# Optimization experiments

Measured on AMD Instinct MI355X. Metric: run time of the kernel, lower is better.

Reference implementation:

```python
import jax, jax.numpy as jnp
import numpy as np

DIM_BODY = 10
DIM_OBJECT = 15
NB_OBJECTS = 3
FIRST_INDS = np.array([0,1,2,3,4,5,6,7,8,9,10,11,12,13,15,16,17,20,21,25])
SECOND_INDS = np.array([0,1,2,3,4,5,6,7,8,9,14,18,19,22,23,24,26,27,28,29])
LOG_SIG_MIN, LOG_SIG_MAX = -20.0, 2.0


def setup_inputs() -> dict:
    key = jax.random.key(0)
    ks = jax.random.split(key, 16)
    B = 65536
    s = 0.05  # weight scale, keeps activations sane
    return {
        "obs": jax.random.normal(ks[0], (B, DIM_BODY + NB_OBJECTS * DIM_OBJECT), jnp.float32),
        "ag": jax.random.normal(ks[1], (B, 30), jnp.float32),
        "g": jax.random.normal(ks[2], (B, 30), jnp.float32),
        "phi_w1": jax.random.normal(ks[3], (80, 256), jnp.float32) * s,
        "phi_b1": jnp.zeros((256,), jnp.float32),
        "phi_w2": jax.random.normal(ks[4], (256, 256), jnp.float32) * s,
        "phi_b2": jnp.zeros((256,), jnp.float32),
        "rho_w1": jax.random.normal(ks[5], (256, 256), jnp.float32) * s,
        "rho_b1": jnp.zeros((256,), jnp.float32),
        "mean_w": jax.random.normal(ks[6], (256, 4), jnp.float32) * s,
        "mean_b": jnp.zeros((4,), jnp.float32),
        "logstd_w": jax.random.normal(ks[7], (256, 4), jnp.float32) * s,
        "logstd_b": jnp.zeros((4,), jnp.float32),
    }


def reference(obs, ag, g, phi_w1, phi_b1, phi_w2, phi_b2, rho_w1, rho_b1,
              mean_w, mean_b, logstd_w, logstd_b):
    body = obs[:, :DIM_BODY]  # [B,10]
    objs = [obs[:, DIM_BODY + DIM_OBJECT * i: DIM_BODY + DIM_OBJECT * (i + 1)]
            for i in range(NB_OBJECTS)]
    ag_f, g_f = ag[:, FIRST_INDS], g[:, FIRST_INDS]
    ag_s, g_s = ag[:, SECOND_INDS], g[:, SECOND_INDS]
    pair_inputs = []
    for i in range(NB_OBJECTS):
        for j in range(NB_OBJECTS):
            if i < j:
                pair_inputs.append(jnp.concatenate([ag_f, body, g_f, objs[i], objs[j]], axis=1))
            elif j < i:
                pair_inputs.append(jnp.concatenate([ag_s, body, g_s, objs[i], objs[j]], axis=1))
    inp = jnp.stack(pair_inputs)  # [6, B, 80]
    # shared phi MLP (2 layers, ReLU on both)
    h = jax.nn.relu(jnp.einsum('pbi,ih->pbh', inp, phi_w1) + phi_b1)
    phi = jax.nn.relu(jnp.einsum('pbh,ho->pbo', h, phi_w2) + phi_b2)
    agg = phi.sum(axis=0)  # [B, 256] sum over pairs
    # rho head
    hr = jax.nn.relu(agg @ rho_w1 + rho_b1)
    mean = hr @ mean_w + mean_b
    logstd = jnp.clip(hr @ logstd_w + logstd_b, LOG_SIG_MIN, LOG_SIG_MAX)
    return mean, logstd
```

## Files before the change

kernel.cpp:

```cpp
#include <hip/hip_runtime.h>
#include <hip/hip_bf16.h>


#define B_TOTAL 65536
#define TROWS   64
#define RSTR    136

typedef __attribute__((ext_vector_type(8))) short s8v;
typedef __attribute__((ext_vector_type(4))) float f4v;

__constant__ int c_PI[6] = {0,0,1,1,2,2};
__constant__ int c_PJ[6] = {1,2,0,2,0,1};
__constant__ int c_PF[6] = {0,0,1,0,1,1};
__constant__ int c_INV[2][30] = {
  {0,1,2,3,4,5,6,7,8,9,10,11,12,13,-1,14,15,16,-1,-1,17,18,-1,-1,-1,19,-1,-1,-1,-1},
  {0,1,2,3,4,5,6,7,8,9,-1,-1,-1,-1,10,-1,-1,-1,11,12,-1,-1,13,14,15,-1,16,17,18,19}};

static __device__ __forceinline__ short bf16s(float v) {
  __hip_bfloat16 h = __float2bfloat16(v);
  union { __hip_bfloat16 h; short s; } u; u.h = h; return u.s;
}

__global__ __launch_bounds__(256)
void prep_weights(const float* __restrict__ phi_w1,
                  const float* __restrict__ phi_b1,
                  const float* __restrict__ phi_w2,
                  const float* __restrict__ rho_w1,
                  const float* __restrict__ mean_w,
                  const float* __restrict__ logstd_w,
                  __hip_bfloat16* __restrict__ W1P,
                  __hip_bfloat16* __restrict__ W2f,
                  __hip_bfloat16* __restrict__ W3f,
                  __hip_bfloat16* __restrict__ W4f) {
  const int wid  = (blockIdx.x * blockDim.x + threadIdx.x) >> 6;
  const int lane = threadIdx.x & 63;
  const int l15  = lane & 15;
  const int kq   = (lane >> 4) * 8;
  if (wid >= 648) return;
  union { short s[8]; s8v v; } o;
  __hip_bfloat16* dst;
  if (wid < 384) {
    const int p = wid >> 6, rem = wid & 63;
    const int nb = rem >> 2, ks = rem & 3;
    const int n = nb * 16 + l15;
    const int f = c_PF[p], oi = c_PI[p], oj = c_PJ[p];
#pragma unroll
    for (int j = 0; j < 8; ++j) {
      int k = ks * 32 + kq + j;
      float v = 0.0f;
      if (k < 30)       { int t = c_INV[f][k];      if (t >= 0) v = phi_w1[t * 256 + n]; }
      else if (k < 60)  { int t = c_INV[f][k - 30]; if (t >= 0) v = phi_w1[(30 + t) * 256 + n]; }
      else if (k < 70)  { v = phi_w1[(20 + k - 60) * 256 + n]; }
      else if (k < 115) { int q = (k - 70) / 15, t = (k - 70) - q * 15;
                          int c = (q == oi) ? 50 + t : (q == oj) ? 65 + t : -1;
                          if (c >= 0) v = phi_w1[c * 256 + n]; }
      else if (k == 115) v = phi_b1[n];
      o.s[j] = bf16s(v);
    }
    dst = W1P + wid * 512 + lane * 8;
  } else if (wid < 512) {
    const int r = wid - 384;
    const int nb = r >> 3, ks = r & 7;
    const int n = nb * 16 + l15;
#pragma unroll
    for (int j = 0; j < 8; ++j)
      o.s[j] = bf16s(phi_w2[(ks * 32 + kq + j) * 256 + n]);
    dst = W2f + r * 512 + lane * 8;
  } else if (wid < 640) {
    const int r = wid - 512;
    const int nb = r >> 3, ks = r & 7;
    const int n = nb * 16 + l15;
#pragma unroll
    for (int j = 0; j < 8; ++j)
      o.s[j] = bf16s(rho_w1[(ks * 32 + kq + j) * 256 + n]);
    dst = W3f + r * 512 + lane * 8;
  } else {
    const int ks = wid - 640;
    const int n = l15;
#pragma unroll
    for (int j = 0; j < 8; ++j) {
      int k = ks * 32 + kq + j;
      float v = (n < 4) ? mean_w[k * 4 + n]
              : (n < 8) ? logstd_w[k * 4 + (n - 4)] : 0.0f;
      o.s[j] = bf16s(v);
    }
    dst = W4f + ks * 512 + lane * 8;
  }
  *reinterpret_cast<s8v*>(dst) = o.v;
}

static __device__ __forceinline__ unsigned pk2(float a, float b) {
  __hip_bfloat162 h = __float22bfloat162_rn(float2{a, b});
  union { __hip_bfloat162 h2; unsigned u; } cv; cv.h2 = h;
  return cv.u;
}

__global__ __launch_bounds__(512, 2)
void actor_main(const float* __restrict__ obs, const float* __restrict__ ag,
                const float* __restrict__ g,
                const __hip_bfloat16* __restrict__ W1P,
                const __hip_bfloat16* __restrict__ W2f,
                const __hip_bfloat16* __restrict__ W3f,
                const __hip_bfloat16* __restrict__ W4f,
                const float* __restrict__ b2, const float* __restrict__ b3,
                const float* __restrict__ meanb,
                const float* __restrict__ logstdb,
                float* __restrict__ out) {
  __shared__ __align__(16) __hip_bfloat16 rawS[TROWS * RSTR];
  __shared__ __align__(16) __hip_bfloat16 HsBuf[2][4 * 8 * 512];

  const int tid  = threadIdx.x;
  const int lane = tid & 63;
  const int w    = tid >> 6;
  const int l15  = lane & 15;
  const int quad = lane >> 4;
  const int r0   = blockIdx.x * TROWS;

  float4 b2v[2];
#pragma unroll
  for (int i = 0; i < 2; ++i)
    b2v[i] = *(const float4*)&b2[w * 32 + i * 16 + quad * 4];

  s8v w2f[8][2];
#pragma unroll
  for (int i = 0; i < 2; ++i)
#pragma unroll
    for (int ks = 0; ks < 8; ++ks)
      w2f[ks][i] = *(const s8v*)&W2f[(((w * 2 + i) * 8 + ks) * 512) + lane * 8];

  {
    const int row = tid >> 3;
    const int c0  = (tid & 7) * 16;
    const float* agr = ag  + (size_t)(r0 + row) * 30;
    const float* gr  = g   + (size_t)(r0 + row) * 30;
    const float* obr = obs + (size_t)(r0 + row) * 55;
    union { short s[16]; s8v v[2]; } o;
#pragma unroll
    for (int cc = 0; cc < 16; ++cc) {
      int c = c0 + cc;
      float v;
      if      (c < 30)  v = agr[c];
      else if (c < 60)  v = gr[c - 30];
      else if (c < 115) v = obr[c - 60];
      else if (c == 115) v = 1.0f;
      else              v = 0.0f;
      o.s[cc] = bf16s(v);
    }
    *reinterpret_cast<s8v*>(&rawS[row * RSTR + c0])     = o.v[0];
    *reinterpret_cast<s8v*>(&rawS[row * RSTR + c0 + 8]) = o.v[1];
  }

  s8v w1c[4][2], w1n[4][2];
#pragma unroll
  for (int i = 0; i < 2; ++i)
#pragma unroll
    for (int ks = 0; ks < 4; ++ks)
      w1c[ks][i] = *(const s8v*)&W1P[(((w * 2 + i) * 4 + ks) * 512) + lane * 8];

  f4v agg[2][4];
#pragma unroll
  for (int i = 0; i < 2; ++i)
#pragma unroll
    for (int rt = 0; rt < 4; ++rt) agg[i][rt] = f4v{0.f, 0.f, 0.f, 0.f};

  const int ebase = l15 * 8 + (quad >> 1) * 128 + (quad & 1) * 4;

  __syncthreads();

#pragma unroll 1
  for (int p = 0; p < 6; ++p) {
    __hip_bfloat16* buf = &HsBuf[p & 1][0];

    if (p < 5) {
      const __hip_bfloat16* nb = W1P + (p + 1) * 32768;
#pragma unroll
      for (int i = 0; i < 2; ++i)
#pragma unroll
        for (int ks = 0; ks < 4; ++ks)
          w1n[ks][i] = *(const s8v*)&nb[(((w * 2 + i) * 4 + ks) * 512) + lane * 8];
    }

    f4v h[2][4];
#pragma unroll
    for (int i = 0; i < 2; ++i)
#pragma unroll
      for (int rt = 0; rt < 4; ++rt) h[i][rt] = f4v{0.f, 0.f, 0.f, 0.f};
#pragma unroll
    for (int ks = 0; ks < 4; ++ks) {
      s8v bx[4];
#pragma unroll
      for (int rt = 0; rt < 4; ++rt)
        bx[rt] = *(const s8v*)&rawS[(rt * 16 + l15) * RSTR + ks * 32 + quad * 8];
#pragma unroll
      for (int i = 0; i < 2; ++i)
#pragma unroll
        for (int rt = 0; rt < 4; ++rt)
          h[i][rt] = __builtin_amdgcn_mfma_f32_16x16x32_bf16(w1c[ks][i], bx[rt], h[i][rt], 0, 0, 0);
    }
#pragma unroll
    for (int i = 0; i < 2; ++i)
#pragma unroll
      for (int rt = 0; rt < 4; ++rt) {
        float v0 = fmaxf(h[i][rt][0], 0.f);
        float v1 = fmaxf(h[i][rt][1], 0.f);
        float v2 = fmaxf(h[i][rt][2], 0.f);
        float v3 = fmaxf(h[i][rt][3], 0.f);
        uint2 U; U.x = pk2(v0, v1); U.y = pk2(v2, v3);
        *reinterpret_cast<uint2*>(&buf[(rt * 8 + w) * 512 + i * 256 + ebase]) = U;
      }
    __syncthreads();

    f4v a2[2][4];
#pragma unroll
    for (int i = 0; i < 2; ++i)
#pragma unroll
      for (int rt = 0; rt < 4; ++rt) a2[i][rt] = f4v{0.f, 0.f, 0.f, 0.f};
#pragma unroll
    for (int ks = 0; ks < 8; ++ks) {
      s8v hf[4];
#pragma unroll
      for (int rt = 0; rt < 4; ++rt)
        hf[rt] = *(const s8v*)&buf[(rt * 8 + ks) * 512 + lane * 8];
#pragma unroll
      for (int i = 0; i < 2; ++i)
#pragma unroll
        for (int rt = 0; rt < 4; ++rt)
          a2[i][rt] = __builtin_amdgcn_mfma_f32_16x16x32_bf16(w2f[ks][i], hf[rt], a2[i][rt], 0, 0, 0);
    }
#pragma unroll
    for (int i = 0; i < 2; ++i)
#pragma unroll
      for (int rt = 0; rt < 4; ++rt) {
        agg[i][rt][0] += fmaxf(a2[i][rt][0] + b2v[i].x, 0.f);
        agg[i][rt][1] += fmaxf(a2[i][rt][1] + b2v[i].y, 0.f);
        agg[i][rt][2] += fmaxf(a2[i][rt][2] + b2v[i].z, 0.f);
        agg[i][rt][3] += fmaxf(a2[i][rt][3] + b2v[i].w, 0.f);
      }

    if (p < 5) {
#pragma unroll
      for (int i = 0; i < 2; ++i)
#pragma unroll
        for (int ks = 0; ks < 4; ++ks)
          w1c[ks][i] = w1n[ks][i];
    }
  }

  s8v w3f[8][2];
#pragma unroll
  for (int i = 0; i < 2; ++i)
#pragma unroll
    for (int ks = 0; ks < 8; ++ks)
      w3f[ks][i] = *(const s8v*)&W3f[(((w * 2 + i) * 8 + ks) * 512) + lane * 8];
  float4 b3v[2];
#pragma unroll
  for (int i = 0; i < 2; ++i)
    b3v[i] = *(const float4*)&b3[w * 32 + i * 16 + quad * 4];

  {
    __hip_bfloat16* bufA = &HsBuf[0][0];
#pragma unroll
    for (int i = 0; i < 2; ++i)
#pragma unroll
      for (int rt = 0; rt < 4; ++rt) {
        uint2 U; U.x = pk2(agg[i][rt][0], agg[i][rt][1]);
        U.y = pk2(agg[i][rt][2], agg[i][rt][3]);
        *reinterpret_cast<uint2*>(&bufA[(rt * 8 + w) * 512 + i * 256 + ebase]) = U;
      }
  }
  __syncthreads();

  f4v a3[2][4];
#pragma unroll
  for (int i = 0; i < 2; ++i)
#pragma unroll
    for (int rt = 0; rt < 4; ++rt) a3[i][rt] = f4v{0.f, 0.f, 0.f, 0.f};
  {
    const __hip_bfloat16* bufA = &HsBuf[0][0];
#pragma unroll
    for (int ks = 0; ks < 8; ++ks) {
      s8v hf[4];
#pragma unroll
      for (int rt = 0; rt < 4; ++rt)
        hf[rt] = *(const s8v*)&bufA[(rt * 8 + ks) * 512 + lane * 8];
#pragma unroll
      for (int i = 0; i < 2; ++i)
#pragma unroll
        for (int rt = 0; rt < 4; ++rt)
          a3[i][rt] = __builtin_amdgcn_mfma_f32_16x16x32_bf16(w3f[ks][i], hf[rt], a3[i][rt], 0, 0, 0);
    }
  }
  {
    __hip_bfloat16* bufB = &HsBuf[1][0];
#pragma unroll
    for (int i = 0; i < 2; ++i)
#pragma unroll
      for (int rt = 0; rt < 4; ++rt) {
        float v0 = fmaxf(a3[i][rt][0] + b3v[i].x, 0.f);
        float v1 = fmaxf(a3[i][rt][1] + b3v[i].y, 0.f);
        float v2 = fmaxf(a3[i][rt][2] + b3v[i].z, 0.f);
        float v3 = fmaxf(a3[i][rt][3] + b3v[i].w, 0.f);
        uint2 U; U.x = pk2(v0, v1); U.y = pk2(v2, v3);
        *reinterpret_cast<uint2*>(&bufB[(rt * 8 + w) * 512 + i * 256 + ebase]) = U;
      }
  }
  __syncthreads();

  if (w < 4) {
    const __hip_bfloat16* bufB = &HsBuf[1][0];
    f4v a4 = f4v{0.f, 0.f, 0.f, 0.f};
#pragma unroll
    for (int ks = 0; ks < 8; ++ks) {
      s8v w4 = *(const s8v*)&W4f[ks * 512 + lane * 8];
      s8v hf = *(const s8v*)&bufB[(w * 8 + ks) * 512 + lane * 8];
      a4 = __builtin_amdgcn_mfma_f32_16x16x32_bf16(w4, hf, a4, 0, 0, 0);
    }
    const int row = r0 + w * 16 + l15;
    if (quad == 0) {
      float4 mb = *(const float4*)meanb;
      float4 o;
      o.x = a4[0] + mb.x; o.y = a4[1] + mb.y;
      o.z = a4[2] + mb.z; o.w = a4[3] + mb.w;
      *reinterpret_cast<float4*>(&out[(size_t)row * 4]) = o;
    } else if (quad == 1) {
      float4 lb = *(const float4*)logstdb;
      float4 o;
      o.x = fminf(fmaxf(a4[0] + lb.x, -20.f), 2.f);
      o.y = fminf(fmaxf(a4[1] + lb.y, -20.f), 2.f);
      o.z = fminf(fmaxf(a4[2] + lb.z, -20.f), 2.f);
      o.w = fminf(fmaxf(a4[3] + lb.w, -20.f), 2.f);
      *reinterpret_cast<float4*>(&out[(size_t)B_TOTAL * 4 + (size_t)row * 4]) = o;
    }
  }
}

extern "C" void kernel_launch(void* const* d_in, const int* in_sizes, int n_in,
                              void* d_out, int out_size, void* d_ws, size_t ws_size,
                              hipStream_t stream) {
  const float* obs      = (const float*)d_in[0];
  const float* ag       = (const float*)d_in[1];
  const float* g        = (const float*)d_in[2];
  const float* phi_w1   = (const float*)d_in[3];
  const float* phi_b1   = (const float*)d_in[4];
  const float* phi_w2   = (const float*)d_in[5];
  const float* phi_b2   = (const float*)d_in[6];
  const float* rho_w1   = (const float*)d_in[7];
  const float* rho_b1   = (const float*)d_in[8];
  const float* mean_w   = (const float*)d_in[9];
  const float* mean_b   = (const float*)d_in[10];
  const float* logstd_w = (const float*)d_in[11];
  const float* logstd_b = (const float*)d_in[12];
  float* out = (float*)d_out;

  char* ws = (char*)d_ws;
  __hip_bfloat16* W1P = (__hip_bfloat16*)(ws);
  __hip_bfloat16* W2f = (__hip_bfloat16*)(ws + 393216);
  __hip_bfloat16* W3f = (__hip_bfloat16*)(ws + 393216 + 131072);
  __hip_bfloat16* W4f = (__hip_bfloat16*)(ws + 393216 + 262144);

  prep_weights<<<162, 256, 0, stream>>>(phi_w1, phi_b1, phi_w2, rho_w1,
                                        mean_w, logstd_w, W1P, W2f, W3f, W4f);
  actor_main<<<B_TOTAL / TROWS, 512, 0, stream>>>(
      obs, ag, g, W1P, W2f, W3f, W4f, phi_b2, rho_b1, mean_b, logstd_b, out);
}
```

Before: 188.9 us.

## Repartition warps into 4 column groups by 2 row halves for phi MLP tiles

Warps now split the output as 4 column groups of 64 features times 2 row halves of 32 rows, where before each warp owned 32 features across all 64 rows. Each warp therefore holds 64 columns of W2/W3 in registers and reads half as many activation fragments from LDS per k-step. W1 is no longer register double-buffered across pairs. Its fragments are now loaded per pair in two halves straight from global memory, which adds load latency inside the loop. Register pressure from the larger W2/W3 fragment arrays also rises, and that may hurt occupancy at 2 blocks per CU.

Result: slower. 222.2 us (+17.6%).

```diff
diff --git a/kernel.cpp b/kernel.cpp
--- a/kernel.cpp
+++ b/kernel.cpp
@@ -112,21 +112,23 @@
   const int tid  = threadIdx.x;
   const int lane = tid & 63;
   const int w    = tid >> 6;
+  const int cg   = w & 3;
+  const int rs   = w >> 2;
   const int l15  = lane & 15;
   const int quad = lane >> 4;
   const int r0   = blockIdx.x * TROWS;
 
-  float4 b2v[2];
-#pragma unroll
-  for (int i = 0; i < 2; ++i)
-    b2v[i] = *(const float4*)&b2[w * 32 + i * 16 + quad * 4];
-
-  s8v w2f[8][2];
-#pragma unroll
-  for (int i = 0; i < 2; ++i)
+  float4 b2v[4];
+#pragma unroll
+  for (int i = 0; i < 4; ++i)
+    b2v[i] = *(const float4*)&b2[cg * 64 + i * 16 + quad * 4];
+
+  s8v w2f[8][4];
+#pragma unroll
+  for (int i = 0; i < 4; ++i)
 #pragma unroll
     for (int ks = 0; ks < 8; ++ks)
-      w2f[ks][i] = *(const s8v*)&W2f[(((w * 2 + i) * 8 + ks) * 512) + lane * 8];
+      w2f[ks][i] = *(const s8v*)&W2f[(((cg * 4 + i) * 8 + ks) * 512) + lane * 8];
 
   {
     const int row = tid >> 3;
@@ -150,18 +152,11 @@
     *reinterpret_cast<s8v*>(&rawS[row * RSTR + c0 + 8]) = o.v[1];
   }
 
-  s8v w1c[4][2], w1n[4][2];
-#pragma unroll
-  for (int i = 0; i < 2; ++i)
-#pragma unroll
-    for (int ks = 0; ks < 4; ++ks)
-      w1c[ks][i] = *(const s8v*)&W1P[(((w * 2 + i) * 4 + ks) * 512) + lane * 8];
-
-  f4v agg[2][4];
-#pragma unroll
-  for (int i = 0; i < 2; ++i)
-#pragma unroll
-    for (int rt = 0; rt < 4; ++rt) agg[i][rt] = f4v{0.f, 0.f, 0.f, 0.f};
+  f4v agg[4][2];
+#pragma unroll
+  for (int i = 0; i < 4; ++i)
+#pragma unroll
+    for (int rt = 0; rt < 2; ++rt) agg[i][rt] = f4v{0.f, 0.f, 0.f, 0.f};
 
   const int ebase = l15 * 8 + (quad >> 1) * 128 + (quad & 1) * 4;
 
@@ -170,138 +165,134 @@
 #pragma unroll 1
   for (int p = 0; p < 6; ++p) {
     __hip_bfloat16* buf = &HsBuf[p & 1][0];
-
-    if (p < 5) {
-      const __hip_bfloat16* nb = W1P + (p + 1) * 32768;
-#pragma unroll
-      for (int i = 0; i < 2; ++i)
+    const __hip_bfloat16* w1base = W1P + p * 32768;
+
+#pragma unroll 1
+    for (int ih = 0; ih < 2; ++ih) {
+      s8v w1f[4][2];
+#pragma unroll
+      for (int il = 0; il < 2; ++il)
 #pragma unroll
         for (int ks = 0; ks < 4; ++ks)
-          w1n[ks][i] = *(const s8v*)&nb[(((w * 2 + i) * 4 + ks) * 512) + lane * 8];
-    }
-
-    f4v h[2][4];
-#pragma unroll
-    for (int i = 0; i < 2; ++i)
-#pragma unroll
-      for (int rt = 0; rt < 4; ++rt) h[i][rt] = f4v{0.f, 0.f, 0.f, 0.f};
-#pragma unroll
-    for (int ks = 0; ks < 4; ++ks) {
-      s8v bx[4];
-#pragma unroll
-      for (int rt = 0; rt < 4; ++rt)
-        bx[rt] = *(const s8v*)&rawS[(rt * 16 + l15) * RSTR + ks * 32 + quad * 8];
-#pragma unroll
-      for (int i = 0; i < 2; ++i)
-#pragma unroll
-        for (int rt = 0; rt < 4; ++rt)
-          h[i][rt] = __builtin_amdgcn_mfma_f32_16x16x32_bf16(w1c[ks][i], bx[rt], h[i][rt], 0, 0, 0);
-    }
-#pragma unroll
-    for (int i = 0; i < 2; ++i)
-#pragma unroll
-      for (int rt = 0; rt < 4; ++rt) {
-        float v0 = fmaxf(h[i][rt][0], 0.f);
-        float v1 = fmaxf(h[i][rt][1], 0.f);
-        float v2 = fmaxf(h[i][rt][2], 0.f);
-        float v3 = fmaxf(h[i][rt][3], 0.f);
-        uint2 U; U.x = pk2(v0, v1); U.y = pk2(v2, v3);
-        *reinterpret_cast<uint2*>(&buf[(rt * 8 + w) * 512 + i * 256 + ebase]) = U;
+          w1f[ks][il] = *(const s8v*)&w1base[(((cg * 4 + ih * 2 + il) * 4 + ks) * 512) + lane * 8];
+      f4v h[2][2];
+#pragma unroll
+      for (int il = 0; il < 2; ++il)
+#pragma unroll
+        for (int rt = 0; rt < 2; ++rt) h[il][rt] = f4v{0.f, 0.f, 0.f, 0.f};
+#pragma unroll
+      for (int ks = 0; ks < 4; ++ks) {
+        s8v bx[2];
+#pragma unroll
+        for (int rt = 0; rt < 2; ++rt)
+          bx[rt] = *(const s8v*)&rawS[((rs * 2 + rt) * 16 + l15) * RSTR + ks * 32 + quad * 8];
+#pragma unroll
+        for (int il = 0; il < 2; ++il)
+#pragma unroll
+          for (int rt = 0; rt < 2; ++rt)
+            h[il][rt] = __builtin_amdgcn_mfma_f32_16x16x32_bf16(w1f[ks][il], bx[rt], h[il][rt], 0, 0, 0);
       }
+#pragma unroll
+      for (int il = 0; il < 2; ++il)
+#pragma unroll
+        for (int rt = 0; rt < 2; ++rt) {
+          float v0 = fmaxf(h[il][rt][0], 0.f);
+          float v1 = fmaxf(h[il][rt][1], 0.f);
+          float v2 = fmaxf(h[il][rt][2], 0.f);
+          float v3 = fmaxf(h[il][rt][3], 0.f);
+          uint2 U; U.x = pk2(v0, v1); U.y = pk2(v2, v3);
+          *reinterpret_cast<uint2*>(
+            &buf[((rs * 2 + rt) * 8 + cg * 2 + ih) * 512 + il * 256 + ebase]) = U;
+        }
+    }
     __syncthreads();
 
-    f4v a2[2][4];
-#pragma unroll
-    for (int i = 0; i < 2; ++i)
-#pragma unroll
-      for (int rt = 0; rt < 4; ++rt) a2[i][rt] = f4v{0.f, 0.f, 0.f, 0.f};
+    f4v a2[4][2];
+#pragma unroll
+    for (int i = 0; i < 4; ++i)
+#pragma unroll
+      for (int rt = 0; rt < 2; ++rt) a2[i][rt] = f4v{0.f, 0.f, 0.f, 0.f};
 #pragma unroll
     for (int ks = 0; ks < 8; ++ks) {
-      s8v hf[4];
-#pragma unroll
-      for (int rt = 0; rt < 4; ++rt)
-        hf[rt] = *(const s8v*)&buf[(rt * 8 + ks) * 512 + lane * 8];
-#pragma unroll
-      for (int i = 0; i < 2; ++i)
-#pragma unroll
-        for (int rt = 0; rt < 4; ++rt)
+      s8v hf[2];
+#pragma unroll
+      for (int rt = 0; rt < 2; ++rt)
+        hf[rt] = *(const s8v*)&buf[((rs * 2 + rt) * 8 + ks) * 512 + lane * 8];
+#pragma unroll
+      for (int i = 0; i < 4; ++i)
+#pragma unroll
+        for (int rt = 0; rt < 2; ++rt)
           a2[i][rt] = __builtin_amdgcn_mfma_f32_16x16x32_bf16(w2f[ks][i], hf[rt], a2[i][rt], 0, 0, 0);
     }
 #pragma unroll
-    for (int i = 0; i < 2; ++i)
-#pragma unroll
-      for (int rt = 0; rt < 4; ++rt) {
+    for (int i = 0; i < 4; ++i)
+#pragma unroll
+      for (int rt = 0; rt < 2; ++rt) {
         agg[i][rt][0] += fmaxf(a2[i][rt][0] + b2v[i].x, 0.f);
         agg[i][rt][1] += fmaxf(a2[i][rt][1] + b2v[i].y, 0.f);
         agg[i][rt][2] += fmaxf(a2[i][rt][2] + b2v[i].z, 0.f);
         agg[i][rt][3] += fmaxf(a2[i][rt][3] + b2v[i].w, 0.f);
       }
-
-    if (p < 5) {
-#pragma unroll
-      for (int i = 0; i < 2; ++i)
-#pragma unroll
-        for (int ks = 0; ks < 4; ++ks)
-          w1c[ks][i] = w1n[ks][i];
-    }
-  }
-
-  s8v w3f[8][2];
-#pragma unroll
-  for (int i = 0; i < 2; ++i)
+  }
+
+  s8v w3f[8][4];
+#pragma unroll
+  for (int i = 0; i < 4; ++i)
 #pragma unroll
     for (int ks = 0; ks < 8; ++ks)
-      w3f[ks][i] = *(const s8v*)&W3f[(((w * 2 + i) * 8 + ks) * 512) + lane * 8];
-  float4 b3v[2];
-#pragma unroll
-  for (int i = 0; i < 2; ++i)
-    b3v[i] = *(const float4*)&b3[w * 32 + i * 16 + quad * 4];
+      w3f[ks][i] = *(const s8v*)&W3f[(((cg * 4 + i) * 8 + ks) * 512) + lane * 8];
+  float4 b3v[4];
+#pragma unroll
+  for (int i = 0; i < 4; ++i)
+    b3v[i] = *(const float4*)&b3[cg * 64 + i * 16 + quad * 4];
 
   {
     __hip_bfloat16* bufA = &HsBuf[0][0];
 #pragma unroll
-    for (int i = 0; i < 2; ++i)
-#pragma unroll
-      for (int rt = 0; rt < 4; ++rt) {
+    for (int i = 0; i < 4; ++i)
+#pragma unroll
+      for (int rt = 0; rt < 2; ++rt) {
         uint2 U; U.x = pk2(agg[i][rt][0], agg[i][rt][1]);
         U.y = pk2(agg[i][rt][2], agg[i][rt][3]);
-        *reinterpret_cast<uint2*>(&bufA[(rt * 8 + w) * 512 + i * 256 + ebase]) = U;
+        *reinterpret_cast<uint2*>(
+          &bufA[((rs * 2 + rt) * 8 + cg * 2 + (i >> 1)) * 512 + (i & 1) * 256 + ebase]) = U;
       }
   }
   __syncthreads();
 
-  f4v a3[2][4];
-#pragma unroll
-  for (int i = 0; i < 2; ++i)
-#pragma unroll
-    for (int rt = 0; rt < 4; ++rt) a3[i][rt] = f4v{0.f, 0.f, 0.f, 0.f};
+  f4v a3[4][2];
+#pragma unroll
+  for (int i = 0; i < 4; ++i)
+#pragma unroll
+    for (int rt = 0; rt < 2; ++rt) a3[i][rt] = f4v{0.f, 0.f, 0.f, 0.f};
   {
     const __hip_bfloat16* bufA = &HsBuf[0][0];
 #pragma unroll
     for (int ks = 0; ks < 8; ++ks) {
-      s8v hf[4];
-#pragma unroll
-      for (int rt = 0; rt < 4; ++rt)
-        hf[rt] = *(const s8v*)&bufA[(rt * 8 + ks) * 512 + lane * 8];
-#pragma unroll
-      for (int i = 0; i < 2; ++i)
-#pragma unroll
-        for (int rt = 0; rt < 4; ++rt)
+      s8v hf[2];
+#pragma unroll
+      for (int rt = 0; rt < 2; ++rt)
+        hf[rt] = *(const s8v*)&bufA[((rs * 2 + rt) * 8 + ks) * 512 + lane * 8];
+#pragma unroll
+      for (int i = 0; i < 4; ++i)
+#pragma unroll
+        for (int rt = 0; rt < 2; ++rt)
           a3[i][rt] = __builtin_amdgcn_mfma_f32_16x16x32_bf16(w3f[ks][i], hf[rt], a3[i][rt], 0, 0, 0);
     }
   }
   {
     __hip_bfloat16* bufB = &HsBuf[1][0];
 #pragma unroll
-    for (int i = 0; i < 2; ++i)
-#pragma unroll
-      for (int rt = 0; rt < 4; ++rt) {
+    for (int i = 0; i < 4; ++i)
+#pragma unroll
+      for (int rt = 0; rt < 2; ++rt) {
         float v0 = fmaxf(a3[i][rt][0] + b3v[i].x, 0.f);
         float v1 = fmaxf(a3[i][rt][1] + b3v[i].y, 0.f);
         float v2 = fmaxf(a3[i][rt][2] + b3v[i].z, 0.f);
         float v3 = fmaxf(a3[i][rt][3] + b3v[i].w, 0.f);
         uint2 U; U.x = pk2(v0, v1); U.y = pk2(v2, v3);
-        *reinterpret_cast<uint2*>(&bufB[(rt * 8 + w) * 512 + i * 256 + ebase]) = U;
+        *reinterpret_cast<uint2*>(
+          &bufB[((rs * 2 + rt) * 8 + cg * 2 + (i >> 1)) * 512 + (i & 1) * 256 + ebase]) = U;
       }
   }
   __syncthreads();
```
